# Kernel optimization log

Measured on AMD Instinct MI355X. Metric: run time of the kernel, lower is better.

The kernel has to match this reference:

```python
import jax, jax.numpy as jnp
import numpy as np

EMBED = 768
HEADS = 12
HEAD_DIM = EMBED // HEADS
HIDDEN = 4 * EMBED
B, N = 8, 1024
EPS = 1e-5


def layernorm(x, g, b):
    mu = jnp.mean(x, axis=-1, keepdims=True)
    var = jnp.var(x, axis=-1, keepdims=True)
    return (x - mu) * jax.lax.rsqrt(var + EPS) * g + b


def setup_inputs() -> dict:
    key = jax.random.key(0)
    ks = jax.random.split(key, 8)
    s_qkv = 1.0 / np.sqrt(EMBED)
    s_fc1 = 1.0 / np.sqrt(EMBED)
    s_fc2 = 1.0 / np.sqrt(HIDDEN)
    return {
        "x": jax.random.normal(ks[0], (B, N, EMBED), dtype=jnp.float32),
        "ln1_g": jnp.ones((EMBED,), jnp.float32),
        "ln1_b": jnp.zeros((EMBED,), jnp.float32),
        "qkv_w": jax.random.uniform(ks[1], (3 * EMBED, EMBED), jnp.float32, -s_qkv, s_qkv),
        "qkv_b": jnp.zeros((3 * EMBED,), jnp.float32),
        "proj_w": jax.random.uniform(ks[2], (EMBED, EMBED), jnp.float32, -s_qkv, s_qkv),
        "proj_b": jnp.zeros((EMBED,), jnp.float32),
        "ln2_g": jnp.ones((EMBED,), jnp.float32),
        "ln2_b": jnp.zeros((EMBED,), jnp.float32),
        "fc1_w": jax.random.uniform(ks[3], (HIDDEN, EMBED), jnp.float32, -s_fc1, s_fc1),
        "fc1_b": jnp.zeros((HIDDEN,), jnp.float32),
        "fc2_w": jax.random.uniform(ks[4], (EMBED, HIDDEN), jnp.float32, -s_fc2, s_fc2),
        "fc2_b": jnp.zeros((EMBED,), jnp.float32),
    }


def reference(x, ln1_g, ln1_b, qkv_w, qkv_b, proj_w, proj_b,
              ln2_g, ln2_b, fc1_w, fc1_b, fc2_w, fc2_b):
    b, n, d = x.shape
    # --- attention sublayer ---
    h = layernorm(x, ln1_g, ln1_b)
    qkv = h @ qkv_w.T + qkv_b                      # [b,n,3d]
    qkv = qkv.reshape(b, n, 3, HEADS, HEAD_DIM).transpose(2, 0, 3, 1, 4)
    q, k, v = qkv[0], qkv[1], qkv[2]               # [b,h,n,hd]
    scores = jnp.einsum('bhqd,bhkd->bhqk', q, k) * (HEAD_DIM ** -0.5)
    attn = jax.nn.softmax(scores, axis=-1)
    ctx = jnp.einsum('bhqk,bhkd->bhqd', attn, v)   # [b,h,n,hd]
    ctx = ctx.transpose(0, 2, 1, 3).reshape(b, n, d)
    x = x + (ctx @ proj_w.T + proj_b)
    # --- MLP sublayer ---
    h = layernorm(x, ln2_g, ln2_b)
    h = jax.nn.gelu(h @ fc1_w.T + fc1_b, approximate=False)
    x = x + (h @ fc2_w.T + fc2_b)
    return x
```

## Files before the change

kernel.cpp:

```cpp
#include <hip/hip_runtime.h>
#include <cstdint>

typedef __bf16 bf16_t;
typedef __attribute__((ext_vector_type(8))) __bf16 bf16x8;
typedef __attribute__((ext_vector_type(4))) __bf16 bf16x4;
typedef __attribute__((ext_vector_type(4))) float f32x4;

#define MFMA16(a, b, c) __builtin_amdgcn_mfma_f32_16x16x32_bf16((a), (b), (c), 0, 0, 0)

__device__ inline float gelu_f(float v) {
    const float u = v + 0.044715f * v * v * v;
    return v / (1.0f + exp2f(-2.3022038f * u));
}

__global__ __launch_bounds__(256) void cvt4_kernel(const float* __restrict__ s0, bf16_t* __restrict__ d0,
                                                   const float* __restrict__ s1, bf16_t* __restrict__ d1,
                                                   const float* __restrict__ s2, bf16_t* __restrict__ d2,
                                                   const float* __restrict__ s3, bf16_t* __restrict__ d3) {
    const int blk = blockIdx.x;
    const float* s; bf16_t* d; int base;
    if (blk < 864)       { s = s0; d = d0; base = blk; }
    else if (blk < 1152) { s = s1; d = d1; base = blk - 864; }
    else if (blk < 2304) { s = s2; d = d2; base = blk - 1152; }
    else                 { s = s3; d = d3; base = blk - 2304; }
    const int i = (base * 256 + threadIdx.x) * 8;
    const float4* sp = (const float4*)(s + i);
    float4 a = sp[0], b = sp[1];
    bf16x8 o;
    o[0] = (bf16_t)a.x; o[1] = (bf16_t)a.y; o[2] = (bf16_t)a.z; o[3] = (bf16_t)a.w;
    o[4] = (bf16_t)b.x; o[5] = (bf16_t)b.y; o[6] = (bf16_t)b.z; o[7] = (bf16_t)b.w;
    *(bf16x8*)(d + i) = o;
}

__global__ __launch_bounds__(256) void ln_kernel(const float* __restrict__ x,
                                                 const float* __restrict__ gw,
                                                 const float* __restrict__ bw,
                                                 bf16_t* __restrict__ out) {
    const int row  = blockIdx.x * 4 + (threadIdx.x >> 6);
    const int lane = threadIdx.x & 63;
    const float4* xr = (const float4*)(x + (long)row * 768);
    float4 v[3];
    float s = 0.f, q = 0.f;
#pragma unroll
    for (int j = 0; j < 3; ++j) {
        v[j] = xr[j * 64 + lane];
        s += v[j].x + v[j].y + v[j].z + v[j].w;
        q += v[j].x * v[j].x + v[j].y * v[j].y + v[j].z * v[j].z + v[j].w * v[j].w;
    }
#pragma unroll
    for (int off = 32; off > 0; off >>= 1) {
        s += __shfl_xor(s, off);
        q += __shfl_xor(q, off);
    }
    const float mu = s * (1.0f / 768.0f);
    const float rs = rsqrtf(q * (1.0f / 768.0f) - mu * mu + 1e-5f);
#pragma unroll
    for (int j = 0; j < 3; ++j) {
        float4 g4 = ((const float4*)gw)[j * 64 + lane];
        float4 b4 = ((const float4*)bw)[j * 64 + lane];
        bf16x4 o;
        o[0] = (bf16_t)((v[j].x - mu) * rs * g4.x + b4.x);
        o[1] = (bf16_t)((v[j].y - mu) * rs * g4.y + b4.y);
        o[2] = (bf16_t)((v[j].z - mu) * rs * g4.z + b4.z);
        o[3] = (bf16_t)((v[j].w - mu) * rs * g4.w + b4.w);
        *(bf16x4*)(out + (long)row * 768 + (j * 64 + lane) * 4) = o;
    }
}

template <int MODE, int NC, int RPX>
__global__ __launch_bounds__(256) void gemm_bt(const bf16_t* __restrict__ A,
                                               const bf16_t* __restrict__ Bw,
                                               const float* __restrict__ bias,
                                               bf16_t* __restrict__ outb,
                                               bf16_t* __restrict__ o1,
                                               bf16_t* __restrict__ o2,
                                               int Nn, int K) {
    __shared__ __align__(16) bf16_t As[128 * 32];
    __shared__ __align__(16) bf16_t Bs[128 * 32];
    __shared__ __align__(16) bf16_t Ts[4 * 16 * 72];
    const int id = blockIdx.x;
    const int xcd = id & 7, sblk = id >> 3;
    const int tn = (sblk % NC) * 128;
    const int tm = (xcd * RPX + sblk / NC) * 128;
    const int w = threadIdx.x >> 6, l = threadIdx.x & 63;
    const int quad = l >> 4, r16 = l & 15;
    const int wm = (w >> 1) * 64, wn = (w & 1) * 64;
    f32x4 acc[4][4] = {};
    const bf16_t* ga = A  + (long)(tm + w * 32 + (l >> 2)) * K + (l & 3) * 8;
    const bf16_t* gb = Bw + (long)(tn + w * 32 + (l >> 2)) * K + (l & 3) * 8;
    bf16_t* la = As + w * 1024;
    bf16_t* lb = Bs + w * 1024;

    bf16x8 pa0 = *(const bf16x8*)(ga);
    bf16x8 pa1 = *(const bf16x8*)(ga + 16 * K);
    bf16x8 pb0 = *(const bf16x8*)(gb);
    bf16x8 pb1 = *(const bf16x8*)(gb + 16 * K);

    for (int k0 = 0; k0 < K; k0 += 32) {
        __syncthreads();
        *(bf16x8*)(la + l * 8)       = pa0;
        *(bf16x8*)(la + 512 + l * 8) = pa1;
        *(bf16x8*)(lb + l * 8)       = pb0;
        *(bf16x8*)(lb + 512 + l * 8) = pb1;
        __syncthreads();
        if (k0 + 32 < K) {
            pa0 = *(const bf16x8*)(ga + k0 + 32);
            pa1 = *(const bf16x8*)(ga + 16 * K + k0 + 32);
            pb0 = *(const bf16x8*)(gb + k0 + 32);
            pb1 = *(const bf16x8*)(gb + 16 * K + k0 + 32);
        }
        bf16x8 af[4], bfr[4];
#pragma unroll
        for (int i = 0; i < 4; ++i) {
            af[i]  = *(const bf16x8*)&As[(wm + i * 16 + r16) * 32 + quad * 8];
            bfr[i] = *(const bf16x8*)&Bs[(wn + i * 16 + r16) * 32 + quad * 8];
        }
#pragma unroll
        for (int i = 0; i < 4; ++i)
#pragma unroll
            for (int j = 0; j < 4; ++j)
                acc[i][j] = MFMA16(af[i], bfr[j], acc[i][j]);
    }

    bf16_t* tw = Ts + w * 16 * 72;
    if (MODE == 0) {
        const int sect = (tn + wn) / 768;
        const int cwb  = tn + wn - sect * 768;
        const int h    = cwb >> 6;
        if (sect == 2) {
#pragma unroll
            for (int i = 0; i < 4; ++i) {
                const int r0 = tm + wm + i * 16 + quad * 4;
                const int b = r0 >> 10, n0 = r0 & 1023;
#pragma unroll
                for (int j = 0; j < 4; ++j) {
                    const int d = j * 16 + r16;
                    const float bv = bias[tn + wn + j * 16 + r16];
                    bf16_t* dst = o2 + ((long)(b * 12 + h) * 64 + d) * 1024;
#pragma unroll
                    for (int rr = 0; rr < 4; ++rr) {
                        const int nn = n0 + rr;
                        const int c = ((nn & 15) << 3) | ((nn >> 4) & 7);
                        dst[(nn & 0x380) + c] = (bf16_t)(acc[i][j][rr] + bv);
                    }
                }
            }
        } else {
            bf16_t* dstbuf = (sect == 0 ? outb : o1);
#pragma unroll
            for (int i = 0; i < 4; ++i) {
#pragma unroll
                for (int j = 0; j < 4; ++j) {
                    const float bv = bias[tn + wn + j * 16 + r16];
#pragma unroll
                    for (int rr = 0; rr < 4; ++rr)
                        tw[(quad * 4 + rr) * 72 + j * 16 + r16] = (bf16_t)(acc[i][j][rr] + bv);
                }
                const int tok = tm + wm + i * 16 + (l >> 2);
                const int b = tok >> 10, n0 = tok & 1023;
                const long base = (long)(b * 12 + h) * 65536 + (long)n0 * 64;
#pragma unroll
                for (int it = 0; it < 2; ++it) {
                    bf16x8 vv = *(const bf16x8*)&tw[(l >> 2) * 72 + (l & 3) * 8 + it * 32];
                    *(bf16x8*)(dstbuf + base + (l & 3) * 8 + it * 32) = vv;
                }
            }
        }
    } else {
#pragma unroll
        for (int i = 0; i < 4; ++i) {
#pragma unroll
            for (int j = 0; j < 4; ++j) {
                const float bv = bias[tn + wn + j * 16 + r16];
#pragma unroll
                for (int rr = 0; rr < 4; ++rr)
                    tw[(quad * 4 + rr) * 72 + j * 16 + r16] = (bf16_t)gelu_f(acc[i][j][rr] + bv);
            }
            const int grow = tm + wm + i * 16 + (l >> 2);
#pragma unroll
            for (int it = 0; it < 2; ++it) {
                bf16x8 vv = *(const bf16x8*)&tw[(l >> 2) * 72 + (l & 3) * 8 + it * 32];
                *(bf16x8*)(outb + (long)grow * Nn + tn + wn + (l & 3) * 8 + it * 32) = vv;
            }
        }
    }
}

__global__ __launch_bounds__(256) void gemm_res64(const bf16_t* __restrict__ A,
                                                  const bf16_t* __restrict__ Bw,
                                                  const float* __restrict__ bias,
                                                  const float* __restrict__ res,
                                                  float* __restrict__ outf,
                                                  int Nn, int K) {
    __shared__ __align__(16) bf16_t As[64 * 32];
    __shared__ __align__(16) bf16_t Bs[128 * 32];
    __shared__ __align__(16) float  Tf[4 * 16 * 68];
    const int id = blockIdx.x;
    const int xcd = id & 7, sblk = id >> 3;
    const int tn = (sblk % 6) * 128;
    const int tm = (xcd * 16 + sblk / 6) * 64;
    const int w = threadIdx.x >> 6, l = threadIdx.x & 63;
    const int quad = l >> 4, r16 = l & 15;
    const int wm = (w >> 1) * 32, wn = (w & 1) * 64;
    f32x4 acc[2][4] = {};
    const bf16_t* ga = A  + (long)(tm + w * 16 + (l >> 2)) * K + (l & 3) * 8;
    const bf16_t* gb = Bw + (long)(tn + w * 32 + (l >> 2)) * K + (l & 3) * 8;
    bf16_t* la = As + w * 512;
    bf16_t* lb = Bs + w * 1024;

    bf16x8 pa = *(const bf16x8*)(ga);
    bf16x8 pb0 = *(const bf16x8*)(gb);
    bf16x8 pb1 = *(const bf16x8*)(gb + 16 * K);

    for (int k0 = 0; k0 < K; k0 += 32) {
        __syncthreads();
        *(bf16x8*)(la + l * 8)       = pa;
        *(bf16x8*)(lb + l * 8)       = pb0;
        *(bf16x8*)(lb + 512 + l * 8) = pb1;
        __syncthreads();
        if (k0 + 32 < K) {
            pa  = *(const bf16x8*)(ga + k0 + 32);
            pb0 = *(const bf16x8*)(gb + k0 + 32);
            pb1 = *(const bf16x8*)(gb + 16 * K + k0 + 32);
        }
        bf16x8 af[2], bfr[4];
#pragma unroll
        for (int i = 0; i < 2; ++i)
            af[i]  = *(const bf16x8*)&As[(wm + i * 16 + r16) * 32 + quad * 8];
#pragma unroll
        for (int j = 0; j < 4; ++j)
            bfr[j] = *(const bf16x8*)&Bs[(wn + j * 16 + r16) * 32 + quad * 8];
#pragma unroll
        for (int i = 0; i < 2; ++i)
#pragma unroll
            for (int j = 0; j < 4; ++j)
                acc[i][j] = MFMA16(af[i], bfr[j], acc[i][j]);
    }
    float* tf = Tf + w * 16 * 68;
#pragma unroll
    for (int i = 0; i < 2; ++i) {
#pragma unroll
        for (int j = 0; j < 4; ++j) {
            const float bv = bias[tn + wn + j * 16 + r16];
#pragma unroll
            for (int rr = 0; rr < 4; ++rr)
                tf[(quad * 4 + rr) * 68 + j * 16 + r16] = acc[i][j][rr] + bv;
        }
        const int grow = tm + wm + i * 16 + (l >> 2);
#pragma unroll
        for (int it = 0; it < 4; ++it) {
            const int gcol = tn + wn + (l & 3) * 4 + it * 16;
            f32x4 vv = *(const f32x4*)&tf[(l >> 2) * 68 + (l & 3) * 4 + it * 16];
            const float4 rv = *(const float4*)(res + (long)grow * Nn + gcol);
            float4 ov;
            ov.x = rv.x + vv[0]; ov.y = rv.y + vv[1];
            ov.z = rv.z + vv[2]; ov.w = rv.w + vv[3];
            *(float4*)(outf + (long)grow * Nn + gcol) = ov;
        }
    }
}

__global__ __launch_bounds__(256, 3) void attn_kernel(const bf16_t* __restrict__ qh,
                                                      const bf16_t* __restrict__ kh,
                                                      const bf16_t* __restrict__ vt,
                                                      bf16_t* __restrict__ ctx) {
    __shared__ __align__(16) bf16_t Ks[128 * 72];
    __shared__ __align__(16) bf16_t Vt[64 * 136];
    __shared__ __align__(16) bf16_t Ps[4 * 16 * 136];
    const int w = threadIdx.x >> 6, l = threadIdx.x & 63;
    const int quad = l >> 4, r16 = l & 15;
    const int bh = blockIdx.x, qt = blockIdx.y;
    const bf16_t* qp = qh + (long)bh * 65536;
    const bf16_t* kp = kh + (long)bh * 65536;
    const bf16_t* vp = vt + (long)bh * 65536;
    const int q0 = qt * 128 + w * 32;
    const float SC = 0.18033688011f;

    bf16x8 qf[2][2];
#pragma unroll
    for (int mt = 0; mt < 2; ++mt)
#pragma unroll
        for (int kq = 0; kq < 2; ++kq)
            qf[mt][kq] = *(const bf16x8*)(qp + (long)(q0 + mt * 16 + r16) * 64 + kq * 32 + quad * 8);

    float lsum[2][4] = {};
    f32x4 oacc[2][4] = {};
    bf16_t* pw = Ps + w * 16 * 136;

    bf16x8 kpre[4], vpre[4];
#pragma unroll
    for (int c = 0; c < 4; ++c) {
        const int cc = threadIdx.x + c * 256;
        kpre[c] = *(const bf16x8*)(kp + (long)(cc >> 3) * 64 + (cc & 7) * 8);
        vpre[c] = *(const bf16x8*)(vp + (long)(cc >> 4) * 1024 + (cc & 15) * 8);
    }

    for (int kt = 0; kt < 8; ++kt) {
        __syncthreads();
#pragma unroll
        for (int c = 0; c < 4; ++c) {
            const int cc = threadIdx.x + c * 256;
            *(bf16x8*)&Ks[(cc >> 3) * 72 + (cc & 7) * 8] = kpre[c];
            *(bf16x8*)&Vt[(cc >> 4) * 136 + (cc & 15) * 8] = vpre[c];
        }
        __syncthreads();
        if (kt < 7) {
            const int kb = (kt + 1) * 128;
#pragma unroll
            for (int c = 0; c < 4; ++c) {
                const int cc = threadIdx.x + c * 256;
                kpre[c] = *(const bf16x8*)(kp + (long)(kb + (cc >> 3)) * 64 + (cc & 7) * 8);
                vpre[c] = *(const bf16x8*)(vp + (long)(cc >> 4) * 1024 + kb + (cc & 15) * 8);
            }
        }

#pragma unroll
        for (int mt = 0; mt < 2; ++mt) {
            f32x4 s[8] = {};
#pragma unroll
            for (int nt = 0; nt < 8; ++nt) {
                bf16x8 kf0 = *(const bf16x8*)&Ks[(nt * 16 + r16) * 72 + quad * 8];
                bf16x8 kf1 = *(const bf16x8*)&Ks[(nt * 16 + r16) * 72 + 32 + quad * 8];
                s[nt] = MFMA16(qf[mt][0], kf0, s[nt]);
                s[nt] = MFMA16(qf[mt][1], kf1, s[nt]);
            }
#pragma unroll
            for (int rr = 0; rr < 4; ++rr) {
                bf16x8 pv;
#pragma unroll
                for (int nt = 0; nt < 8; ++nt) {
                    const float p = exp2f(s[nt][rr] * SC);
                    lsum[mt][rr] += p;
                    pv[nt] = (bf16_t)p;
                }
                *(bf16x8*)&pw[(quad * 4 + rr) * 136 + r16 * 8] = pv;
            }
#pragma unroll
            for (int kc = 0; kc < 4; ++kc) {
                bf16x8 pf = *(const bf16x8*)&pw[r16 * 136 + kc * 32 + quad * 8];
#pragma unroll
                for (int dt = 0; dt < 4; ++dt) {
                    bf16x8 vf = *(const bf16x8*)&Vt[(dt * 16 + r16) * 136 + kc * 32 + quad * 8];
                    oacc[mt][dt] = MFMA16(pf, vf, oacc[mt][dt]);
                }
            }
        }
    }
#pragma unroll
    for (int mt = 0; mt < 2; ++mt)
#pragma unroll
        for (int rr = 0; rr < 4; ++rr) {
#pragma unroll
            for (int off = 1; off < 16; off <<= 1)
                lsum[mt][rr] += __shfl_xor(lsum[mt][rr], off);
        }
    const int b = bh / 12, h = bh % 12;
    const long tb = (long)b * 1024;
#pragma unroll
    for (int mt = 0; mt < 2; ++mt) {
#pragma unroll
        for (int dt = 0; dt < 4; ++dt)
#pragma unroll
            for (int rr = 0; rr < 4; ++rr)
                pw[(quad * 4 + rr) * 72 + dt * 16 + r16] =
                    (bf16_t)(oacc[mt][dt][rr] / lsum[mt][rr]);
        const int tok = q0 + mt * 16 + (l >> 2);
        const int off = (l & 3) * 16;
        bf16_t* dst = ctx + (tb + tok) * 768 + h * 64 + off;
        const bf16_t* src = &pw[(l >> 2) * 72 + off];
#pragma unroll
        for (int it = 0; it < 2; ++it)
            *(bf16x8*)(dst + it * 8) = *(const bf16x8*)(src + it * 8);
    }
}

extern "C" void kernel_launch(void* const* d_in, const int* in_sizes, int n_in,
                              void* d_out, int out_size, void* d_ws, size_t ws_size,
                              hipStream_t stream) {
    const float* x      = (const float*)d_in[0];
    const float* ln1_g  = (const float*)d_in[1];
    const float* ln1_b  = (const float*)d_in[2];
    const float* qkv_w  = (const float*)d_in[3];
    const float* qkv_b  = (const float*)d_in[4];
    const float* proj_w = (const float*)d_in[5];
    const float* proj_b = (const float*)d_in[6];
    const float* ln2_g  = (const float*)d_in[7];
    const float* ln2_b  = (const float*)d_in[8];
    const float* fc1_w  = (const float*)d_in[9];
    const float* fc1_b  = (const float*)d_in[10];
    const float* fc2_w  = (const float*)d_in[11];
    const float* fc2_b  = (const float*)d_in[12];

    char* p = (char*)d_ws;
    bf16_t* wqkv  = (bf16_t*)p; p += (size_t)2304 * 768 * 2;
    bf16_t* wproj = (bf16_t*)p; p += (size_t)768 * 768 * 2;
    bf16_t* wfc1  = (bf16_t*)p; p += (size_t)3072 * 768 * 2;
    bf16_t* wfc2  = (bf16_t*)p; p += (size_t)768 * 3072 * 2;
    bf16_t* h1    = (bf16_t*)p; p += (size_t)8192 * 768 * 2;
    bf16_t* qhb   = (bf16_t*)p; p += (size_t)96 * 1024 * 64 * 2;
    bf16_t* khb   = (bf16_t*)p; p += (size_t)96 * 1024 * 64 * 2;
    bf16_t* vtb   = (bf16_t*)p; p += (size_t)96 * 64 * 1024 * 2;
    bf16_t* ctx   = (bf16_t*)p; p += (size_t)8192 * 768 * 2;
    float*  x2    = (float*)p;  p += (size_t)8192 * 768 * 4;
    bf16_t* h2    = (bf16_t*)p; p += (size_t)8192 * 768 * 2;
    bf16_t* a1    = (bf16_t*)p; p += (size_t)8192 * 3072 * 2;

    cvt4_kernel<<<3456, 256, 0, stream>>>(qkv_w, wqkv, proj_w, wproj, fc1_w, wfc1, fc2_w, wfc2);

    ln_kernel<<<2048, 256, 0, stream>>>(x, ln1_g, ln1_b, h1);
    gemm_bt<0, 18, 8><<<1152, 256, 0, stream>>>(h1, wqkv, qkv_b, qhb, khb, vtb, 2304, 768);
    attn_kernel<<<dim3(96, 8), 256, 0, stream>>>(qhb, khb, vtb, ctx);
    gemm_res64<<<768, 256, 0, stream>>>(ctx, wproj, proj_b, x, x2, 768, 768);
    ln_kernel<<<2048, 256, 0, stream>>>(x2, ln2_g, ln2_b, h2);
    gemm_bt<2, 24, 8><<<1536, 256, 0, stream>>>(h2, wfc1, fc1_b, a1, nullptr, nullptr, 3072, 768);
    gemm_res64<<<768, 256, 0, stream>>>(a1, wfc2, fc2_b, x2, (float*)d_out, 768, 3072);
}
```

Before: 376.5 us.

## Use direct global-to-LDS loads with double-buffered shared tiles in GEMMs

Both GEMM kernels now fetch their A and B tiles with global_load_lds, which writes straight into shared memory, in place of loading into registers and storing to LDS afterwards. Shared tiles are double-buffered, so the next K-slice is fetched while MFMAs run on the current one, and one barrier per iteration is dropped. This removes the register staging and the LDS write instructions. In exchange it doubles LDS use per block, which can lower occupancy, and it waits on vmcnt(0) at the top of each iteration.

```diff
diff --git a/kernel.cpp b/kernel.cpp
--- a/kernel.cpp
+++ b/kernel.cpp
@@ -7,6 +7,10 @@
 typedef __attribute__((ext_vector_type(4))) float f32x4;
 
 #define MFMA16(a, b, c) __builtin_amdgcn_mfma_f32_16x16x32_bf16((a), (b), (c), 0, 0, 0)
+
+#define GLOAD16(g, l) __builtin_amdgcn_global_load_lds(                      \
+    (const __attribute__((address_space(1))) void*)(g),                      \
+    (__attribute__((address_space(3))) void*)(l), 16, 0, 0)
 
 __device__ inline float gelu_f(float v) {
     const float u = v + 0.044715f * v * v * v;
@@ -75,8 +79,8 @@
                                                bf16_t* __restrict__ o1,
                                                bf16_t* __restrict__ o2,
                                                int Nn, int K) {
-    __shared__ __align__(16) bf16_t As[128 * 32];
-    __shared__ __align__(16) bf16_t Bs[128 * 32];
+    __shared__ __align__(16) bf16_t As[2][128 * 32];
+    __shared__ __align__(16) bf16_t Bs[2][128 * 32];
     __shared__ __align__(16) bf16_t Ts[4 * 16 * 72];
     const int id = blockIdx.x;
     const int xcd = id & 7, sblk = id >> 3;
@@ -88,38 +92,37 @@
     f32x4 acc[4][4] = {};
     const bf16_t* ga = A  + (long)(tm + w * 32 + (l >> 2)) * K + (l & 3) * 8;
     const bf16_t* gb = Bw + (long)(tn + w * 32 + (l >> 2)) * K + (l & 3) * 8;
-    bf16_t* la = As + w * 1024;
-    bf16_t* lb = Bs + w * 1024;
-
-    bf16x8 pa0 = *(const bf16x8*)(ga);
-    bf16x8 pa1 = *(const bf16x8*)(ga + 16 * K);
-    bf16x8 pb0 = *(const bf16x8*)(gb);
-    bf16x8 pb1 = *(const bf16x8*)(gb + 16 * K);
-
+    const int lw = w * 1024;
+
+    GLOAD16(ga,          &As[0][lw]);
+    GLOAD16(ga + 16 * K, &As[0][lw + 512]);
+    GLOAD16(gb,          &Bs[0][lw]);
+    GLOAD16(gb + 16 * K, &Bs[0][lw + 512]);
+
+    int cur = 0;
     for (int k0 = 0; k0 < K; k0 += 32) {
-        __syncthreads();
-        *(bf16x8*)(la + l * 8)       = pa0;
-        *(bf16x8*)(la + 512 + l * 8) = pa1;
-        *(bf16x8*)(lb + l * 8)       = pb0;
-        *(bf16x8*)(lb + 512 + l * 8) = pb1;
+        asm volatile("s_waitcnt vmcnt(0)" ::: "memory");
         __syncthreads();
         if (k0 + 32 < K) {
-            pa0 = *(const bf16x8*)(ga + k0 + 32);
-            pa1 = *(const bf16x8*)(ga + 16 * K + k0 + 32);
-            pb0 = *(const bf16x8*)(gb + k0 + 32);
-            pb1 = *(const bf16x8*)(gb + 16 * K + k0 + 32);
+            const bf16_t* gan = ga + k0 + 32;
+            const bf16_t* gbn = gb + k0 + 32;
+            GLOAD16(gan,          &As[cur ^ 1][lw]);
+            GLOAD16(gan + 16 * K, &As[cur ^ 1][lw + 512]);
+            GLOAD16(gbn,          &Bs[cur ^ 1][lw]);
+            GLOAD16(gbn + 16 * K, &Bs[cur ^ 1][lw + 512]);
         }
         bf16x8 af[4], bfr[4];
 #pragma unroll
         for (int i = 0; i < 4; ++i) {
-            af[i]  = *(const bf16x8*)&As[(wm + i * 16 + r16) * 32 + quad * 8];
-            bfr[i] = *(const bf16x8*)&Bs[(wn + i * 16 + r16) * 32 + quad * 8];
+            af[i]  = *(const bf16x8*)&As[cur][(wm + i * 16 + r16) * 32 + quad * 8];
+            bfr[i] = *(const bf16x8*)&Bs[cur][(wn + i * 16 + r16) * 32 + quad * 8];
         }
 #pragma unroll
         for (int i = 0; i < 4; ++i)
 #pragma unroll
             for (int j = 0; j < 4; ++j)
                 acc[i][j] = MFMA16(af[i], bfr[j], acc[i][j]);
+        cur ^= 1;
     }
 
     bf16_t* tw = Ts + w * 16 * 72;
@@ -192,8 +195,8 @@
                                                   const float* __restrict__ res,
                                                   float* __restrict__ outf,
                                                   int Nn, int K) {
-    __shared__ __align__(16) bf16_t As[64 * 32];
-    __shared__ __align__(16) bf16_t Bs[128 * 32];
+    __shared__ __align__(16) bf16_t As[2][64 * 32];
+    __shared__ __align__(16) bf16_t Bs[2][128 * 32];
     __shared__ __align__(16) float  Tf[4 * 16 * 68];
     const int id = blockIdx.x;
     const int xcd = id & 7, sblk = id >> 3;
@@ -205,36 +208,36 @@
     f32x4 acc[2][4] = {};
     const bf16_t* ga = A  + (long)(tm + w * 16 + (l >> 2)) * K + (l & 3) * 8;
     const bf16_t* gb = Bw + (long)(tn + w * 32 + (l >> 2)) * K + (l & 3) * 8;
-    bf16_t* la = As + w * 512;
-    bf16_t* lb = Bs + w * 1024;
-
-    bf16x8 pa = *(const bf16x8*)(ga);
-    bf16x8 pb0 = *(const bf16x8*)(gb);
-    bf16x8 pb1 = *(const bf16x8*)(gb + 16 * K);
-
+    const int lwa = w * 512, lwb = w * 1024;
+
+    GLOAD16(ga,          &As[0][lwa]);
+    GLOAD16(gb,          &Bs[0][lwb]);
+    GLOAD16(gb + 16 * K, &Bs[0][lwb + 512]);
+
+    int cur = 0;
     for (int k0 = 0; k0 < K; k0 += 32) {
-        __syncthreads();
-        *(bf16x8*)(la + l * 8)       = pa;
-        *(bf16x8*)(lb + l * 8)       = pb0;
-        *(bf16x8*)(lb + 512 + l * 8) = pb1;
+        asm volatile("s_waitcnt vmcnt(0)" ::: "memory");
         __syncthreads();
         if (k0 + 32 < K) {
-            pa  = *(const bf16x8*)(ga + k0 + 32);
-            pb0 = *(const bf16x8*)(gb + k0 + 32);
-            pb1 = *(const bf16x8*)(gb + 16 * K + k0 + 32);
+            const bf16_t* gan = ga + k0 + 32;
+            const bf16_t* gbn = gb + k0 + 32;
+            GLOAD16(gan,          &As[cur ^ 1][lwa]);
+            GLOAD16(gbn,          &Bs[cur ^ 1][lwb]);
+            GLOAD16(gbn + 16 * K, &Bs[cur ^ 1][lwb + 512]);
         }
         bf16x8 af[2], bfr[4];
 #pragma unroll
         for (int i = 0; i < 2; ++i)
-            af[i]  = *(const bf16x8*)&As[(wm + i * 16 + r16) * 32 + quad * 8];
+            af[i]  = *(const bf16x8*)&As[cur][(wm + i * 16 + r16) * 32 + quad * 8];
 #pragma unroll
         for (int j = 0; j < 4; ++j)
-            bfr[j] = *(const bf16x8*)&Bs[(wn + j * 16 + r16) * 32 + quad * 8];
+            bfr[j] = *(const bf16x8*)&Bs[cur][(wn + j * 16 + r16) * 32 + quad * 8];
 #pragma unroll
         for (int i = 0; i < 2; ++i)
 #pragma unroll
             for (int j = 0; j < 4; ++j)
                 acc[i][j] = MFMA16(af[i], bfr[j], acc[i][j]);
+        cur ^= 1;
     }
     float* tf = Tf + w * 16 * 68;
 #pragma unroll
```

Result: no change. 379.4 us (+0.8%).
